# Kernel optimization log

Hardware: AMD Instinct MI355X
Metric: run time of the kernel (lower is better)

The kernel has to match this reference:

```python
import jax, jax.numpy as jnp
import numpy as np

HIDDEN = 1024
HEADS = 16
SCALE_EXP = 0.2  # module: scale = hidden_size ** (-scale)


def setup_inputs() -> dict:
    key = jax.random.key(0)
    k1, k2, k3, k4, k5 = jax.random.split(key, 5)
    b, s, h = 2, 2048, HIDDEN
    std = 1.0 / np.sqrt(h)
    return {
        "sequence_embedding": jax.random.normal(k1, (b, s, h), dtype=jnp.float32),
        "kqv_w": jax.random.normal(k2, (h, 3 * h), dtype=jnp.float32) * std,
        "kqv_b": jax.random.normal(k3, (3 * h,), dtype=jnp.float32) * std,
        "ff_w": jax.random.normal(k4, (h, h), dtype=jnp.float32) * std,
        "ff_b": jax.random.normal(k5, (h,), dtype=jnp.float32) * std,
    }


def reference(sequence_embedding, kqv_w, kqv_b, ff_w, ff_b):
    b, s, hid = sequence_embedding.shape
    d = hid // HEADS
    scale = hid ** (-SCALE_EXP)
    kqv = sequence_embedding @ kqv_w + kqv_b  # [b, s, 3h]
    k, q, v = jnp.split(kqv, 3, axis=-1)
    split_heads = lambda x: x.reshape(b, s, HEADS, d).transpose(0, 2, 1, 3)  # b h s d
    k, q, v = split_heads(k), split_heads(q), split_heads(v)
    # scores[s, n] = k_s . q_n  (rows = key pos, cols = query pos)
    scores = jnp.einsum('bhsd,bhnd->bhsn', k, q) * scale
    # faithful to source: softmax over last axis n (the QUERY axis)
    attn = jax.nn.softmax(scores, axis=-1)
    # sum over s (key positions); output indexed by n
    out = jnp.einsum('bhsn,bhsd->bhnd', attn, v)  # [b, h, s, d]
    out = out.transpose(0, 2, 1, 3).reshape(b, s, hid)
    return out @ ff_w + ff_b  # dropout is identity at inference
```

## Files before the change

kernel.cpp:

```cpp
#include <hip/hip_runtime.h>

typedef unsigned short u16;
typedef unsigned int   u32;
typedef __attribute__((ext_vector_type(8))) short s16x8;
typedef __attribute__((ext_vector_type(4))) float f32x4;

#define B_   2
#define S_   2048
#define HID  1024
#define NH   16
#define N3   3072
#define M_   4096
#define SCALE 0.25f
#define STATS_OFF 8.0f

__device__ __forceinline__ u16 f2b(float f) {
  union { float f; u32 u; } v; v.f = f;
  u32 r = (v.u + 0x7FFFu + ((v.u >> 16) & 1u)) >> 16;
  return (u16)r;
}

__global__ __launch_bounds__(256) void conv_bf16(const float* __restrict__ in,
                                                 u16* __restrict__ out, int n4) {
  int i = blockIdx.x * 256 + threadIdx.x;
  if (i >= n4) return;
  float4 v = ((const float4*)in)[i];
  ushort4 o = { f2b(v.x), f2b(v.y), f2b(v.z), f2b(v.w) };
  ((ushort4*)out)[i] = o;
}

__global__ __launch_bounds__(256) void transpose_bf16(const float* __restrict__ in,
                                                      u16* __restrict__ out,
                                                      int K, int N) {
  __shared__ float T[32][33];
  const int t = threadIdx.x;
  const int k0 = blockIdx.y * 32, n0 = blockIdx.x * 32;
  {
    int r = t >> 3, c4 = (t & 7) * 4;
    float4 v = *(const float4*)(in + (size_t)(k0 + r) * N + n0 + c4);
    T[r][c4 + 0] = v.x; T[r][c4 + 1] = v.y; T[r][c4 + 2] = v.z; T[r][c4 + 3] = v.w;
  }
  __syncthreads();
  int n = t >> 3, kc = (t & 7) * 4;
  ushort4 o = { f2b(T[kc + 0][n]), f2b(T[kc + 1][n]), f2b(T[kc + 2][n]), f2b(T[kc + 3][n]) };
  *(ushort4*)(out + (size_t)(n0 + n) * K + k0 + kc) = o;
}

template <int OUTBF16>
__global__ __launch_bounds__(256) void gemm_bf16(const u16* __restrict__ A,
                                                 const u16* __restrict__ Bt,
                                                 const float* __restrict__ bias,
                                                 void* __restrict__ Cout,
                                                 int M, int N, int K) {
  __shared__ u16 Al[128 * 40];
  __shared__ u16 Bl[128 * 40];
  const int t = threadIdx.x, lane = t & 63, w = t >> 6;
  const int m0 = blockIdx.y * 128, n0 = blockIdx.x * 128;
  const int wm = (w >> 1) * 64, wn = (w & 1) * 64;
  const int r = lane & 15, g = lane >> 4;

  f32x4 acc[4][4];
  #pragma unroll
  for (int i = 0; i < 4; ++i)
    #pragma unroll
    for (int j = 0; j < 4; ++j) acc[i][j] = (f32x4){0.f, 0.f, 0.f, 0.f};

  const int row0 = t >> 2, kc0 = t & 3;
  const int row1 = (t + 256) >> 2, kc1 = t & 3;

  for (int k0 = 0; k0 < K; k0 += 32) {
    __syncthreads();
    uint4 a0 = *(const uint4*)(A  + (size_t)(m0 + row0) * K + k0 + kc0 * 8);
    uint4 a1 = *(const uint4*)(A  + (size_t)(m0 + row1) * K + k0 + kc1 * 8);
    uint4 b0 = *(const uint4*)(Bt + (size_t)(n0 + row0) * K + k0 + kc0 * 8);
    uint4 b1 = *(const uint4*)(Bt + (size_t)(n0 + row1) * K + k0 + kc1 * 8);
    *(uint4*)(Al + row0 * 40 + kc0 * 8) = a0;
    *(uint4*)(Al + row1 * 40 + kc1 * 8) = a1;
    *(uint4*)(Bl + row0 * 40 + kc0 * 8) = b0;
    *(uint4*)(Bl + row1 * 40 + kc1 * 8) = b1;
    __syncthreads();

    s16x8 af[4], bf[4];
    #pragma unroll
    for (int mf = 0; mf < 4; ++mf)
      af[mf] = *(const s16x8*)(Al + (wm + mf * 16 + r) * 40 + g * 8);
    #pragma unroll
    for (int nf = 0; nf < 4; ++nf)
      bf[nf] = *(const s16x8*)(Bl + (wn + nf * 16 + r) * 40 + g * 8);
    #pragma unroll
    for (int mf = 0; mf < 4; ++mf)
      #pragma unroll
      for (int nf = 0; nf < 4; ++nf)
        acc[mf][nf] = __builtin_amdgcn_mfma_f32_16x16x32_bf16(af[mf], bf[nf], acc[mf][nf], 0, 0, 0);
  }

  float bv[4];
  #pragma unroll
  for (int nf = 0; nf < 4; ++nf) bv[nf] = bias[n0 + wn + nf * 16 + r];

  #pragma unroll
  for (int mf = 0; mf < 4; ++mf)
    #pragma unroll
    for (int nf = 0; nf < 4; ++nf)
      #pragma unroll
      for (int q = 0; q < 4; ++q) {
        float o = acc[mf][nf][q] + bv[nf];
        size_t idx = (size_t)(m0 + wm + mf * 16 + 4 * g + q) * N + (n0 + wn + nf * 16 + r);
        if (OUTBF16) ((u16*)Cout)[idx] = f2b(o);
        else         ((float*)Cout)[idx] = o;
      }
}

__global__ __launch_bounds__(256) void attn_stats(const u16* __restrict__ kqv,
                                                  float* __restrict__ L) {
  __shared__ u16 Kl[64 * 72];
  __shared__ u16 Ql[64 * 72];
  const int t = threadIdx.x, lane = t & 63, w = t >> 6;
  const int bh = blockIdx.y, b = bh >> 4, h = bh & 15;
  const int s0 = blockIdx.x * 64;
  const u16* base = kqv + (size_t)b * S_ * N3;
  const int r = lane & 15, g = lane >> 4;

  {
    int c = t;       int row = c >> 3, dc = c & 7;
    *(uint4*)(Kl + row * 72 + dc * 8) =
        *(const uint4*)(base + (size_t)(s0 + row) * N3 + h * 64 + dc * 8);
    c = t + 256;     row = c >> 3; dc = c & 7;
    *(uint4*)(Kl + row * 72 + dc * 8) =
        *(const uint4*)(base + (size_t)(s0 + row) * N3 + h * 64 + dc * 8);
  }

  float z[4] = {0.f, 0.f, 0.f, 0.f};

  for (int nt = 0; nt < 32; ++nt) {
    const int n0 = nt * 64;
    __syncthreads();
    {
      int c = t;       int row = c >> 3, dc = c & 7;
      *(uint4*)(Ql + row * 72 + dc * 8) =
          *(const uint4*)(base + (size_t)(n0 + row) * N3 + HID + h * 64 + dc * 8);
      c = t + 256;     row = c >> 3; dc = c & 7;
      *(uint4*)(Ql + row * 72 + dc * 8) =
          *(const uint4*)(base + (size_t)(n0 + row) * N3 + HID + h * 64 + dc * 8);
    }
    __syncthreads();

    s16x8 ka0 = *(const s16x8*)(Kl + (w * 16 + r) * 72 + g * 8);
    s16x8 ka1 = *(const s16x8*)(Kl + (w * 16 + r) * 72 + 32 + g * 8);
    #pragma unroll
    for (int nf = 0; nf < 4; ++nf) {
      f32x4 sc = (f32x4){0.f, 0.f, 0.f, 0.f};
      s16x8 qb0 = *(const s16x8*)(Ql + (nf * 16 + r) * 72 + g * 8);
      s16x8 qb1 = *(const s16x8*)(Ql + (nf * 16 + r) * 72 + 32 + g * 8);
      sc = __builtin_amdgcn_mfma_f32_16x16x32_bf16(ka0, qb0, sc, 0, 0, 0);
      sc = __builtin_amdgcn_mfma_f32_16x16x32_bf16(ka1, qb1, sc, 0, 0, 0);
      #pragma unroll
      for (int q = 0; q < 4; ++q)
        z[q] += __expf(sc[q] * SCALE - STATS_OFF);
    }
  }
  #pragma unroll
  for (int m = 1; m <= 8; m <<= 1)
    #pragma unroll
    for (int q = 0; q < 4; ++q) z[q] += __shfl_xor(z[q], m);
  if (r == 0)
    #pragma unroll
    for (int q = 0; q < 4; ++q)
      L[(size_t)bh * S_ + s0 + w * 16 + 4 * g + q] = STATS_OFF + __logf(z[q]);
}

__global__ __launch_bounds__(256) void attn_pv(const u16* __restrict__ kqv,
                                               const float* __restrict__ L,
                                               u16* __restrict__ attn) {
  __shared__ u16 Ql[64 * 72];
  __shared__ u16 Kl[64 * 72];
  __shared__ u16 Vt[64 * 72];
  __shared__ u16 Pl[64 * 72];
  const int t = threadIdx.x, lane = t & 63, w = t >> 6;
  const int bh = blockIdx.y, b = bh >> 4, h = bh & 15;
  const int n0 = blockIdx.x * 64;
  const u16* base = kqv + (size_t)b * S_ * N3;
  const float* Lb = L + (size_t)bh * S_;
  const int r = lane & 15, g = lane >> 4;

  {
    int c = t;       int row = c >> 3, dc = c & 7;
    *(uint4*)(Ql + row * 72 + dc * 8) =
        *(const uint4*)(base + (size_t)(n0 + row) * N3 + HID + h * 64 + dc * 8);
    c = t + 256;     row = c >> 3; dc = c & 7;
    *(uint4*)(Ql + row * 72 + dc * 8) =
        *(const uint4*)(base + (size_t)(n0 + row) * N3 + HID + h * 64 + dc * 8);
  }
  __syncthreads();
  const s16x8 qa0 = *(const s16x8*)(Ql + (w * 16 + r) * 72 + g * 8);
  const s16x8 qa1 = *(const s16x8*)(Ql + (w * 16 + r) * 72 + 32 + g * 8);

  f32x4 oacc[4];
  #pragma unroll
  for (int i = 0; i < 4; ++i) oacc[i] = (f32x4){0.f, 0.f, 0.f, 0.f};

  const int vdc = t & 7, vp = t >> 3;
  const int vpb = (vp >> 2) ^ vdc;
  const int vso = 2 * (vp & 3);

  for (int st = 0; st < 32; ++st) {
    const int s0 = st * 64;
    __syncthreads();
    {
      int c = t;       int row = c >> 3, dc = c & 7;
      *(uint4*)(Kl + row * 72 + dc * 8) =
          *(const uint4*)(base + (size_t)(s0 + row) * N3 + h * 64 + dc * 8);
      c = t + 256;     row = c >> 3; dc = c & 7;
      *(uint4*)(Kl + row * 72 + dc * 8) =
          *(const uint4*)(base + (size_t)(s0 + row) * N3 + h * 64 + dc * 8);
    }
    {
      uint4 v0 = *(const uint4*)(base + (size_t)(s0 + 2 * vp)     * N3 + 2 * HID + h * 64 + vdc * 8);
      uint4 v1 = *(const uint4*)(base + (size_t)(s0 + 2 * vp + 1) * N3 + 2 * HID + h * 64 + vdc * 8);
      const u16* e0 = (const u16*)&v0;
      const u16* e1 = (const u16*)&v1;
      #pragma unroll
      for (int i = 0; i < 8; ++i) {
        u32 pk = (u32)e0[i] | ((u32)e1[i] << 16);
        *(u32*)(Vt + (vdc * 8 + i) * 72 + vpb * 8 + vso) = pk;
      }
    }
    __syncthreads();

    float Lv[4];
    #pragma unroll
    for (int sf = 0; sf < 4; ++sf) Lv[sf] = Lb[s0 + sf * 16 + r];
    #pragma unroll
    for (int sf = 0; sf < 4; ++sf) {
      f32x4 sc = (f32x4){0.f, 0.f, 0.f, 0.f};
      s16x8 kb0 = *(const s16x8*)(Kl + (sf * 16 + r) * 72 + g * 8);
      s16x8 kb1 = *(const s16x8*)(Kl + (sf * 16 + r) * 72 + 32 + g * 8);
      sc = __builtin_amdgcn_mfma_f32_16x16x32_bf16(qa0, kb0, sc, 0, 0, 0);
      sc = __builtin_amdgcn_mfma_f32_16x16x32_bf16(qa1, kb1, sc, 0, 0, 0);
      #pragma unroll
      for (int q = 0; q < 4; ++q) {
        u16 pw = f2b(__expf(sc[q] * SCALE - Lv[sf]));
        Pl[(w * 16 + 4 * g + q) * 72 + sf * 16 + r] = pw;
      }
    }
    #pragma unroll
    for (int ks = 0; ks < 2; ++ks) {
      s16x8 pa = *(const s16x8*)(Pl + (w * 16 + r) * 72 + ks * 32 + g * 8);
      #pragma unroll
      for (int df = 0; df < 4; ++df) {
        int d = df * 16 + r;
        int pb2 = (ks * 4 + g) ^ (d >> 3);
        s16x8 vb = *(const s16x8*)(Vt + d * 72 + pb2 * 8);
        oacc[df] = __builtin_amdgcn_mfma_f32_16x16x32_bf16(pa, vb, oacc[df], 0, 0, 0);
      }
    }
  }

  #pragma unroll
  for (int df = 0; df < 4; ++df)
    #pragma unroll
    for (int q = 0; q < 4; ++q)
      attn[(size_t)(b * S_ + n0 + w * 16 + 4 * g + q) * HID + h * 64 + df * 16 + r] =
          f2b(oacc[df][q]);
}

extern "C" void kernel_launch(void* const* d_in, const int* in_sizes, int n_in,
                              void* d_out, int out_size, void* d_ws, size_t ws_size,
                              hipStream_t stream) {
  const float* x     = (const float*)d_in[0];
  const float* kqv_w = (const float*)d_in[1];
  const float* kqv_b = (const float*)d_in[2];
  const float* ff_w  = (const float*)d_in[3];
  const float* ff_b  = (const float*)d_in[4];
  float* out = (float*)d_out;

  u16* xb    = (u16*)d_ws;
  u16* w1t   = xb   + (size_t)M_ * HID;
  u16* w2t   = w1t  + (size_t)N3 * HID;
  u16* kqvb  = w2t  + (size_t)HID * HID;
  float* Lr  = (float*)(kqvb + (size_t)M_ * N3);
  u16* attnb = (u16*)(Lr + (size_t)B_ * NH * S_);

  dim3 blk(256);
  conv_bf16<<<dim3((M_ * HID / 4 + 255) / 256), blk, 0, stream>>>(x, xb, M_ * HID / 4);
  transpose_bf16<<<dim3(N3 / 32, HID / 32), blk, 0, stream>>>(kqv_w, w1t, HID, N3);
  transpose_bf16<<<dim3(HID / 32, HID / 32), blk, 0, stream>>>(ff_w, w2t, HID, HID);

  gemm_bf16<1><<<dim3(N3 / 128, M_ / 128), blk, 0, stream>>>(
      xb, w1t, kqv_b, kqvb, M_, N3, HID);

  attn_stats<<<dim3(S_ / 64, B_ * NH), blk, 0, stream>>>(kqvb, Lr);
  attn_pv   <<<dim3(S_ / 64, B_ * NH), blk, 0, stream>>>(kqvb, Lr, attnb);

  gemm_bf16<0><<<dim3(HID / 128, M_ / 128), blk, 0, stream>>>(
      attnb, w2t, ff_b, out, M_, HID, HID);
}
```

Baseline: 190.3 us.

## Use global_load_lds in GEMM, pre-transpose V, exp2 softmax, packed bf16 convert

The GEMM tile loads now use direct global-to-LDS loads with an unpadded 32-wide LDS layout, so data no longer passes through registers. V is transposed once into a global buffer by a new kernel, which lets attn_pv load V tiles contiguously instead of shuffling them inside the loop. The softmax switches to exp2 with a folded log2e·scale constant, and probabilities are converted with the packed bf16 instruction. The risks are LDS bank conflicts from dropping the padding, plus an extra kernel launch and extra global traffic for the V copy.

New measurement: 208.6 us. 1.1x slower.

```diff
diff --git a/kernel.cpp b/kernel.cpp
--- a/kernel.cpp
+++ b/kernel.cpp
@@ -11,14 +11,25 @@
 #define NH   16
 #define N3   3072
 #define M_   4096
-#define SCALE 0.25f
-#define STATS_OFF 8.0f
+#define C2   0.36067376022224085f
+#define OFF2 12.0f
 
 __device__ __forceinline__ u16 f2b(float f) {
   union { float f; u32 u; } v; v.f = f;
   u32 r = (v.u + 0x7FFFu + ((v.u >> 16) & 1u)) >> 16;
   return (u16)r;
 }
+
+__device__ __forceinline__ u32 cvt_pk_bf16(float lo, float hi) {
+  u32 r;
+  asm("v_cvt_pk_bf16_f32 %0, %1, %2" : "=v"(r) : "v"(lo), "v"(hi));
+  return r;
+}
+
+#define GLL(gp, lp)                                                          \
+  __builtin_amdgcn_global_load_lds(                                          \
+      (const __attribute__((address_space(1))) void*)(gp),                   \
+      (__attribute__((address_space(3))) void*)(lp), 16, 0, 0)
 
 __global__ __launch_bounds__(256) void conv_bf16(const float* __restrict__ in,
                                                  u16* __restrict__ out, int n4) {
@@ -46,14 +57,43 @@
   *(ushort4*)(out + (size_t)(n0 + n) * K + k0 + kc) = o;
 }
 
+__global__ __launch_bounds__(256) void v_transpose(const u16* __restrict__ kqv,
+                                                   u16* __restrict__ Vtg) {
+  __shared__ u16 Vl[64 * 66];
+  const int t = threadIdx.x;
+  const int bh = blockIdx.y, b = bh >> 4, h = bh & 15;
+  const int s0 = blockIdx.x * 64;
+  const u16* src = kqv + (size_t)b * S_ * N3 + 2 * HID + h * 64;
+  #pragma unroll
+  for (int cc = 0; cc < 2; ++cc) {
+    int c = t + cc * 256;
+    int row = c >> 3, dc = c & 7;
+    uint4 v = *(const uint4*)(src + (size_t)(s0 + row) * N3 + dc * 8);
+    u32* pe = (u32*)&v;
+    #pragma unroll
+    for (int e = 0; e < 4; ++e)
+      *(u32*)(Vl + row * 66 + dc * 8 + 2 * e) = pe[e];
+  }
+  __syncthreads();
+  #pragma unroll
+  for (int cc = 0; cc < 2; ++cc) {
+    int c = t + cc * 256;
+    int d = c >> 3, sc = c & 7;
+    u16 tmp[8];
+    #pragma unroll
+    for (int j = 0; j < 8; ++j) tmp[j] = Vl[(sc * 8 + j) * 66 + d];
+    *(uint4*)(Vtg + ((size_t)bh * 64 + d) * S_ + s0 + sc * 8) = *(uint4*)tmp;
+  }
+}
+
 template <int OUTBF16>
 __global__ __launch_bounds__(256) void gemm_bf16(const u16* __restrict__ A,
                                                  const u16* __restrict__ Bt,
                                                  const float* __restrict__ bias,
                                                  void* __restrict__ Cout,
                                                  int M, int N, int K) {
-  __shared__ u16 Al[128 * 40];
-  __shared__ u16 Bl[128 * 40];
+  __shared__ u16 Al[128 * 32];
+  __shared__ u16 Bl[128 * 32];
   const int t = threadIdx.x, lane = t & 63, w = t >> 6;
   const int m0 = blockIdx.y * 128, n0 = blockIdx.x * 128;
   const int wm = (w >> 1) * 64, wn = (w & 1) * 64;
@@ -65,28 +105,25 @@
     #pragma unroll
     for (int j = 0; j < 4; ++j) acc[i][j] = (f32x4){0.f, 0.f, 0.f, 0.f};
 
-  const int row0 = t >> 2, kc0 = t & 3;
-  const int row1 = (t + 256) >> 2, kc1 = t & 3;
+  const int c0 = (w << 7) + lane, c1 = c0 + 64;
+  const int ar0 = c0 >> 2, ak0 = (c0 & 3) << 3;
+  const int ar1 = c1 >> 2, ak1 = (c1 & 3) << 3;
 
   for (int k0 = 0; k0 < K; k0 += 32) {
     __syncthreads();
-    uint4 a0 = *(const uint4*)(A  + (size_t)(m0 + row0) * K + k0 + kc0 * 8);
-    uint4 a1 = *(const uint4*)(A  + (size_t)(m0 + row1) * K + k0 + kc1 * 8);
-    uint4 b0 = *(const uint4*)(Bt + (size_t)(n0 + row0) * K + k0 + kc0 * 8);
-    uint4 b1 = *(const uint4*)(Bt + (size_t)(n0 + row1) * K + k0 + kc1 * 8);
-    *(uint4*)(Al + row0 * 40 + kc0 * 8) = a0;
-    *(uint4*)(Al + row1 * 40 + kc1 * 8) = a1;
-    *(uint4*)(Bl + row0 * 40 + kc0 * 8) = b0;
-    *(uint4*)(Bl + row1 * 40 + kc1 * 8) = b1;
+    GLL(A  + (size_t)(m0 + ar0) * K + k0 + ak0, Al + (w << 10));
+    GLL(A  + (size_t)(m0 + ar1) * K + k0 + ak1, Al + (w << 10) + 512);
+    GLL(Bt + (size_t)(n0 + ar0) * K + k0 + ak0, Bl + (w << 10));
+    GLL(Bt + (size_t)(n0 + ar1) * K + k0 + ak1, Bl + (w << 10) + 512);
     __syncthreads();
 
     s16x8 af[4], bf[4];
     #pragma unroll
     for (int mf = 0; mf < 4; ++mf)
-      af[mf] = *(const s16x8*)(Al + (wm + mf * 16 + r) * 40 + g * 8);
+      af[mf] = *(const s16x8*)(Al + (wm + mf * 16 + r) * 32 + g * 8);
     #pragma unroll
     for (int nf = 0; nf < 4; ++nf)
-      bf[nf] = *(const s16x8*)(Bl + (wn + nf * 16 + r) * 40 + g * 8);
+      bf[nf] = *(const s16x8*)(Bl + (wn + nf * 16 + r) * 32 + g * 8);
     #pragma unroll
     for (int mf = 0; mf < 4; ++mf)
       #pragma unroll
@@ -112,7 +149,7 @@
 }
 
 __global__ __launch_bounds__(256) void attn_stats(const u16* __restrict__ kqv,
-                                                  float* __restrict__ L) {
+                                                  float* __restrict__ L2) {
   __shared__ u16 Kl[64 * 72];
   __shared__ u16 Ql[64 * 72];
   const int t = threadIdx.x, lane = t & 63, w = t >> 6;
@@ -156,7 +193,7 @@
       sc = __builtin_amdgcn_mfma_f32_16x16x32_bf16(ka1, qb1, sc, 0, 0, 0);
       #pragma unroll
       for (int q = 0; q < 4; ++q)
-        z[q] += __expf(sc[q] * SCALE - STATS_OFF);
+        z[q] += exp2f(fmaf(sc[q], C2, -OFF2));
     }
   }
   #pragma unroll
@@ -166,21 +203,23 @@
   if (r == 0)
     #pragma unroll
     for (int q = 0; q < 4; ++q)
-      L[(size_t)bh * S_ + s0 + w * 16 + 4 * g + q] = STATS_OFF + __logf(z[q]);
+      L2[(size_t)bh * S_ + s0 + w * 16 + 4 * g + q] = OFF2 + log2f(z[q]);
 }
 
 __global__ __launch_bounds__(256) void attn_pv(const u16* __restrict__ kqv,
-                                               const float* __restrict__ L,
+                                               const u16* __restrict__ Vtg,
+                                               const float* __restrict__ L2,
                                                u16* __restrict__ attn) {
   __shared__ u16 Ql[64 * 72];
   __shared__ u16 Kl[64 * 72];
-  __shared__ u16 Vt[64 * 72];
+  __shared__ u16 Vl[64 * 72];
   __shared__ u16 Pl[64 * 72];
   const int t = threadIdx.x, lane = t & 63, w = t >> 6;
   const int bh = blockIdx.y, b = bh >> 4, h = bh & 15;
   const int n0 = blockIdx.x * 64;
   const u16* base = kqv + (size_t)b * S_ * N3;
-  const float* Lb = L + (size_t)bh * S_;
+  const u16* vtb  = Vtg + (size_t)bh * 64 * S_;
+  const float* Lb = L2 + (size_t)bh * S_;
   const int r = lane & 15, g = lane >> 4;
 
   {
@@ -199,12 +238,12 @@
   #pragma unroll
   for (int i = 0; i < 4; ++i) oacc[i] = (f32x4){0.f, 0.f, 0.f, 0.f};
 
-  const int vdc = t & 7, vp = t >> 3;
-  const int vpb = (vp >> 2) ^ vdc;
-  const int vso = 2 * (vp & 3);
-
   for (int st = 0; st < 32; ++st) {
     const int s0 = st * 64;
+    float Lv[4];
+    #pragma unroll
+    for (int sf = 0; sf < 4; ++sf) Lv[sf] = Lb[s0 + sf * 16 + r];
+
     __syncthreads();
     {
       int c = t;       int row = c >> 3, dc = c & 7;
@@ -215,21 +254,15 @@
           *(const uint4*)(base + (size_t)(s0 + row) * N3 + h * 64 + dc * 8);
     }
     {
-      uint4 v0 = *(const uint4*)(base + (size_t)(s0 + 2 * vp)     * N3 + 2 * HID + h * 64 + vdc * 8);
-      uint4 v1 = *(const uint4*)(base + (size_t)(s0 + 2 * vp + 1) * N3 + 2 * HID + h * 64 + vdc * 8);
-      const u16* e0 = (const u16*)&v0;
-      const u16* e1 = (const u16*)&v1;
-      #pragma unroll
-      for (int i = 0; i < 8; ++i) {
-        u32 pk = (u32)e0[i] | ((u32)e1[i] << 16);
-        *(u32*)(Vt + (vdc * 8 + i) * 72 + vpb * 8 + vso) = pk;
-      }
-    }
-    __syncthreads();
-
-    float Lv[4];
-    #pragma unroll
-    for (int sf = 0; sf < 4; ++sf) Lv[sf] = Lb[s0 + sf * 16 + r];
+      int c = t;       int row = c >> 3, dc = c & 7;
+      *(uint4*)(Vl + row * 72 + dc * 8) =
+          *(const uint4*)(vtb + (size_t)row * S_ + s0 + dc * 8);
+      c = t + 256;     row = c >> 3; dc = c & 7;
+      *(uint4*)(Vl + row * 72 + dc * 8) =
+          *(const uint4*)(vtb + (size_t)row * S_ + s0 + dc * 8);
+    }
+    __syncthreads();
+
     #pragma unroll
     for (int sf = 0; sf < 4; ++sf) {
       f32x4 sc = (f32x4){0.f, 0.f, 0.f, 0.f};
@@ -237,20 +270,24 @@
       s16x8 kb1 = *(const s16x8*)(Kl + (sf * 16 + r) * 72 + 32 + g * 8);
       sc = __builtin_amdgcn_mfma_f32_16x16x32_bf16(qa0, kb0, sc, 0, 0, 0);
       sc = __builtin_amdgcn_mfma_f32_16x16x32_bf16(qa1, kb1, sc, 0, 0, 0);
-      #pragma unroll
-      for (int q = 0; q < 4; ++q) {
-        u16 pw = f2b(__expf(sc[q] * SCALE - Lv[sf]));
-        Pl[(w * 16 + 4 * g + q) * 72 + sf * 16 + r] = pw;
-      }
+      float p0 = exp2f(fmaf(sc[0], C2, -Lv[sf]));
+      float p1 = exp2f(fmaf(sc[1], C2, -Lv[sf]));
+      float p2 = exp2f(fmaf(sc[2], C2, -Lv[sf]));
+      float p3 = exp2f(fmaf(sc[3], C2, -Lv[sf]));
+      u32 pk01 = cvt_pk_bf16(p0, p1);
+      u32 pk23 = cvt_pk_bf16(p2, p3);
+      int pbase = (w * 16 + 4 * g) * 72 + sf * 16 + r;
+      Pl[pbase]           = (u16)pk01;
+      Pl[pbase + 72]      = (u16)(pk01 >> 16);
+      Pl[pbase + 144]     = (u16)pk23;
+      Pl[pbase + 216]     = (u16)(pk23 >> 16);
     }
     #pragma unroll
     for (int ks = 0; ks < 2; ++ks) {
       s16x8 pa = *(const s16x8*)(Pl + (w * 16 + r) * 72 + ks * 32 + g * 8);
       #pragma unroll
       for (int df = 0; df < 4; ++df) {
-        int d = df * 16 + r;
-        int pb2 = (ks * 4 + g) ^ (d >> 3);
-        s16x8 vb = *(const s16x8*)(Vt + d * 72 + pb2 * 8);
+        s16x8 vb = *(const s16x8*)(Vl + (df * 16 + r) * 72 + ks * 32 + g * 8);
         oacc[df] = __builtin_amdgcn_mfma_f32_16x16x32_bf16(pa, vb, oacc[df], 0, 0, 0);
       }
     }
@@ -278,7 +315,8 @@
   u16* w1t   = xb   + (size_t)M_ * HID;
   u16* w2t   = w1t  + (size_t)N3 * HID;
   u16* kqvb  = w2t  + (size_t)HID * HID;
-  float* Lr  = (float*)(kqvb + (size_t)M_ * N3);
+  u16* vtg   = kqvb + (size_t)M_ * N3;
+  float* Lr  = (float*)(vtg + (size_t)B_ * NH * 64 * S_);
   u16* attnb = (u16*)(Lr + (size_t)B_ * NH * S_);
 
   dim3 blk(256);
@@ -289,8 +327,9 @@
   gemm_bf16<1><<<dim3(N3 / 128, M_ / 128), blk, 0, stream>>>(
       xb, w1t, kqv_b, kqvb, M_, N3, HID);
 
-  attn_stats<<<dim3(S_ / 64, B_ * NH), blk, 0, stream>>>(kqvb, Lr);
-  attn_pv   <<<dim3(S_ / 64, B_ * NH), blk, 0, stream>>>(kqvb, Lr, attnb);
+  v_transpose<<<dim3(S_ / 64, B_ * NH), blk, 0, stream>>>(kqvb, vtg);
+  attn_stats <<<dim3(S_ / 64, B_ * NH), blk, 0, stream>>>(kqvb, Lr);
+  attn_pv    <<<dim3(S_ / 64, B_ * NH), blk, 0, stream>>>(kqvb, vtg, Lr, attnb);
 
   gemm_bf16<0><<<dim3(HID / 128, M_ / 128), blk, 0, stream>>>(
       attnb, w2t, ff_b, out, M_, HID, HID);
```
